# Kernel tuning notes

Measured on AMD Instinct MI355X. Metric: run time of the kernel, lower is better.

## Reference

```python
import jax, jax.numpy as jnp
import numpy as np

K_NEIGHBORS = 32  # nsample

def setup_inputs() -> dict:
    key = jax.random.key(0)
    ks = jax.random.split(key, 16)
    B, C, N = 4, 3, 4096
    def w(k, shape):
        return jax.random.normal(k, shape, dtype=jnp.float32) * 0.05
    inp = {"x": jax.random.normal(ks[0], (B, C, N), dtype=jnp.float32)}
    # three scale MLPs share shapes -> stack along leading scale axis (s=3)
    inp["sW0"] = w(ks[1], (3, 64, 3));    inp["sb0"] = w(ks[2], (3, 64))
    inp["sW1"] = w(ks[3], (3, 64, 64));   inp["sb1"] = w(ks[4], (3, 64))
    inp["sW2"] = w(ks[5], (3, 128, 64));  inp["sb2"] = w(ks[6], (3, 128))
    inp["gW0"] = w(ks[7], (256, 384));    inp["gb0"] = w(ks[8], (256,))
    inp["gW1"] = w(ks[9], (1024, 256));   inp["gb1"] = w(ks[10], (1024,))
    inp["mW0"] = w(ks[11], (256, 1024));  inp["mb0"] = w(ks[12], (256,))
    inp["mW1"] = w(ks[13], (128, 256));   inp["mb1"] = w(ks[14], (128,))
    return inp

def _knn_idx(x, k):
    # x: [B, 3, N] channels-first points; k nearest neighbors excluding self
    pts = jnp.swapaxes(x, 1, 2)                       # [B, N, 3]
    sq = jnp.sum(pts * pts, axis=-1)                  # [B, N]
    d = sq[:, :, None] + sq[:, None, :] - 2.0 * jnp.einsum('bnc,bmc->bnm', pts, pts)
    _, idx = jax.lax.top_k(-d, k + 1)                 # nearest first (self at 0)
    return idx[:, :, 1:]                              # [B, N, k]

def reference(x, sW0, sb0, sW1, sb1, sW2, sb2, gW0, gb0, gW1, gb1, mW0, mb0, mW1, mb1):
    B, C, N = x.shape
    # radius is unused by sample_and_group_knn -> all three scales share knn idx
    idx = _knn_idx(x, K_NEIGHBORS)                    # [B, N, K]
    # gather: per-batch x[:, idx[b]] -> [B, C, N, K]
    g = jax.vmap(lambda xf, i: xf[:, i])(x, idx)
    # three shared-weight 1x1-conv MLPs, batched over scale axis s
    h = jax.nn.relu(jnp.einsum('bcnk,soc->sbonk', g, sW0) + sb0[:, None, :, None, None])
    h = jax.nn.relu(jnp.einsum('sbcnk,soc->sbonk', h, sW1) + sb1[:, None, :, None, None])
    h = jax.nn.relu(jnp.einsum('sbcnk,soc->sbonk', h, sW2) + sb2[:, None, :, None, None])
    p = jnp.max(h, axis=-1)                           # [3, B, 128, N] max over neighbors
    point = jnp.moveaxis(p, 0, 1).reshape(B, 3 * p.shape[2], N)  # concat scales -> [B, 384, N]
    gf = jax.nn.relu(jnp.einsum('bcn,oc->bon', point, gW0) + gb0[None, :, None])
    gf = jax.nn.relu(jnp.einsum('bcn,oc->bon', gf, gW1) + gb1[None, :, None])     # [B,1024,N]
    msf = jax.nn.relu(jnp.einsum('bcn,oc->bon', gf, mW0) + mb0[None, :, None])
    msf = jax.nn.relu(jnp.einsum('bcn,oc->bon', msf, mW1) + mb1[None, :, None])   # [B,128,N]
    global_feature = jnp.max(gf, axis=-1)             # [B, 1024]
    return (global_feature, msf)
```

## Files before the change

kernel.cpp:

```cpp
#include <hip/hip_runtime.h>
#include <hip/hip_bf16.h>

#define NPTS 4096
#define KNN  32

typedef __attribute__((ext_vector_type(8))) short short8;
typedef __attribute__((ext_vector_type(4))) float floatx4;
typedef unsigned short u16x2 __attribute__((ext_vector_type(2)));

__device__ __forceinline__ unsigned short f2bf(float f) {
    unsigned u = __float_as_uint(f);
    u = (u + 0x7FFFu + ((u >> 16) & 1u)) >> 16;
    return (unsigned short)u;
}

__global__ __launch_bounds__(256) void prep_all(
    const float* __restrict__ x, float4* __restrict__ pts4,
    const float* __restrict__ gW0, const float* __restrict__ gW1,
    const float* __restrict__ mW0, const float* __restrict__ mW1,
    const float* __restrict__ sW1, const float* __restrict__ sW2,
    unsigned short* __restrict__ Wb0, unsigned short* __restrict__ Wb1,
    unsigned short* __restrict__ Wb2, unsigned short* __restrict__ Wb3,
    unsigned short* __restrict__ Wb4, unsigned short* __restrict__ Wb5)
{
    const int blk = blockIdx.x, t = threadIdx.x;
    if (blk < 64) {
        const int i = blk * 256 + t;
        const int b = i >> 12, n = i & (NPTS - 1);
        const float* xb = x + (size_t)b * 3 * NPTS;
        const float qx = xb[n], qy = xb[NPTS + n], qz = xb[2 * NPTS + n];
        pts4[i] = make_float4(qx, qy, qz, qx * qx + qy * qy + qz * qz);
    } else {
        const int wi = (blk - 64) * 256 + t;
        float v; unsigned short* dst;
        if (wi < 98304)       { v = gW0[wi];          dst = Wb0 + wi; }
        else if (wi < 360448) { v = gW1[wi - 98304];  dst = Wb1 + (wi - 98304); }
        else if (wi < 622592) { v = mW0[wi - 360448]; dst = Wb2 + (wi - 360448); }
        else if (wi < 655360) { v = mW1[wi - 622592]; dst = Wb3 + (wi - 622592); }
        else if (wi < 667648) { v = sW1[wi - 655360]; dst = Wb4 + (wi - 655360); }
        else                  { v = sW2[wi - 667648]; dst = Wb5 + (wi - 667648); }
        *dst = f2bf(v);
    }
}

__global__ __launch_bounds__(256) void knn_kernel15(const float4* __restrict__ pts4,
                                                    int* __restrict__ knn_out)
{
    __shared__ unsigned sredA[2][4], sredB[2][4];
    __shared__ unsigned long long C2[2][256];
    __shared__ unsigned ccnt[2];

    const int t = threadIdx.x, wid = t >> 6, lane = t & 63;
    const int pr = blockIdx.x;
    const int b  = pr >> 11;
    const int qa = (pr & 2047) << 1;
    const int qb = qa + 1;
    const float4* P = pts4 + ((size_t)b << 12);
    const float4 sA = P[qa];
    const float4 sB = P[qb];

    if (t < 2) ccnt[t] = 0u;

    unsigned kA[16], kB[16];
    #pragma unroll
    for (int r = 0; r < 16; ++r) {
        const float4 c = P[(r << 8) + t];
        float dA = (sA.w + c.w) - 2.0f * (sA.x * c.x + sA.y * c.y + sA.z * c.z);
        float dB = (sB.w + c.w) - 2.0f * (sB.x * c.x + sB.y * c.y + sB.z * c.z);
        unsigned uA = __float_as_uint(dA), uB = __float_as_uint(dB);
        kA[r] = (uA & 0x80000000u) ? ~uA : (uA | 0x80000000u);
        kB[r] = (uB & 0x80000000u) ? ~uB : (uB | 0x80000000u);
    }

    int pp = 0;
    auto countLE2 = [&](unsigned ta, unsigned tb, unsigned& ga, unsigned& gb) {
        unsigned ca = 0, cb = 0;
        #pragma unroll
        for (int r = 0; r < 16; ++r) {
            ca += (unsigned)__popcll(__ballot(kA[r] <= ta));
            cb += (unsigned)__popcll(__ballot(kB[r] <= tb));
        }
        if (lane == 0) { sredA[pp & 1][wid] = ca; sredB[pp & 1][wid] = cb; }
        __syncthreads();
        ga = sredA[pp & 1][0] + sredA[pp & 1][1] +
             sredA[pp & 1][2] + sredA[pp & 1][3];
        gb = sredB[pp & 1][0] + sredB[pp & 1][1] +
             sredB[pp & 1][2] + sredB[pp & 1][3];
        ++pp;
    };

    unsigned loA = 0x100u, hiA = 0x1FEu, cHiA = 4096u;
    unsigned loB = 0x100u, hiB = 0x1FEu, cHiB = 4096u;
    for (int it = 0; it < 8; ++it) {
        const unsigned mA = (loA + hiA) >> 1;
        const unsigned mB = (loB + hiB) >> 1;
        unsigned ga, gb;
        countLE2((mA << 23) | 0x7FFFFFu, (mB << 23) | 0x7FFFFFu, ga, gb);
        if (ga >= 33u) { hiA = mA; cHiA = ga; } else loA = mA + 1u;
        if (gb >= 33u) { hiB = mB; cHiB = gb; } else loB = mB + 1u;
    }
    unsigned loKA = loA << 23, hiKA = (loA << 23) | 0x7FFFFFu, cFA = cHiA;
    unsigned loKB = loB << 23, hiKB = (loB << 23) | 0x7FFFFFu, cFB = cHiB;

    while (((cFA > 256u) && (loKA < hiKA)) || ((cFB > 256u) && (loKB < hiKB))) {
        const bool nA = (cFA > 256u) && (loKA < hiKA);
        const bool nB = (cFB > 256u) && (loKB < hiKB);
        const unsigned mA = nA ? (loKA + ((hiKA - loKA) >> 1)) : hiKA;
        const unsigned mB = nB ? (loKB + ((hiKB - loKB) >> 1)) : hiKB;
        unsigned ga, gb;
        countLE2(mA, mB, ga, gb);
        if (nA) { if (ga >= 33u) { hiKA = mA; cFA = ga; } else loKA = mA + 1u; }
        if (nB) { if (gb >= 33u) { hiKB = mB; cFB = gb; } else loKB = mB + 1u; }
    }
    const unsigned thrA = hiKA, thrB = hiKB;

    #pragma unroll
    for (int r = 0; r < 16; ++r) {
        if (kA[r] <= thrA) {
            unsigned p = atomicAdd(&ccnt[0], 1u);
            if (p < 256u)
                C2[0][p] = ((unsigned long long)kA[r] << 32) |
                           (unsigned)((r << 8) + t);
        }
        if (kB[r] <= thrB) {
            unsigned p = atomicAdd(&ccnt[1], 1u);
            if (p < 256u)
                C2[1][p] = ((unsigned long long)kB[r] << 32) |
                           (unsigned)((r << 8) + t);
        }
    }
    __syncthreads();

    int ncA = (int)ccnt[0]; if (ncA > 256) ncA = 256;
    int ncB = (int)ccnt[1]; if (ncB > 256) ncB = 256;
    if (t < ncA) {
        const unsigned long long me = C2[0][t];
        int rank = 0;
        for (int j = 0; j < ncA; ++j) rank += (C2[0][j] < me) ? 1 : 0;
        if (rank >= 1 && rank <= KNN)
            knn_out[((size_t)((b << 12) + qa)) * KNN + (rank - 1)] =
                (int)(me & 0xFFFFFFFFu);
    }
    if (t < ncB) {
        const unsigned long long me = C2[1][t];
        int rank = 0;
        for (int j = 0; j < ncB; ++j) rank += (C2[1][j] < me) ? 1 : 0;
        if (rank >= 1 && rank <= KNN)
            knn_out[((size_t)((b << 12) + qb)) * KNN + (rank - 1)] =
                (int)(me & 0xFFFFFFFFu);
    }
}

__global__ __launch_bounds__(256) void pointmlp_mfma(
    const float* __restrict__ x,
    const float* __restrict__ sW0, const float* __restrict__ sb0,
    const unsigned short* __restrict__ W1b, const float* __restrict__ sb1,
    const unsigned short* __restrict__ W2b, const float* __restrict__ sb2,
    unsigned short* __restrict__ F)
{
    __shared__ __align__(16) unsigned short W1s[64 * 72];
    __shared__ __align__(16) unsigned short W2s[128 * 72];
    __shared__ __align__(16) unsigned short h0T[32 * 72];
    __shared__ __align__(16) unsigned short h1T[32 * 72];
    __shared__ float W0s[192];
    __shared__ float b0s[64], b1s[64], b2s[128];
    __shared__ float pts[3 * 33];

    const int t = threadIdx.x;
    const int s = blockIdx.y;
    const int tile = blockIdx.x;
    const int b = tile >> 7;
    const int j0 = (tile & 127) << 5;
    const float* xb = x + (size_t)b * 3 * NPTS;

    if (t < 192) W0s[t] = sW0[s * 192 + t];
    if (t < 64) b0s[t] = sb0[s * 64 + t];
    if (t >= 64 && t < 128) b1s[t - 64] = sb1[s * 64 + (t - 64)];
    if (t < 128) b2s[t] = sb2[s * 128 + t];
    if (t < 96) { int c = t >> 5, p = t & 31; pts[c * 33 + p] = xb[c * NPTS + j0 + p]; }
    {
        const int o = t & 63, qq = t >> 6;
        const unsigned short* src = W1b + (size_t)s * 4096 + o * 64 + qq * 16;
        *(uint4*)&W1s[o * 72 + qq * 16]     = *(const uint4*)src;
        *(uint4*)&W1s[o * 72 + qq * 16 + 8] = *(const uint4*)(src + 8);
    }
    {
        const int o2 = t & 127, hh = t >> 7;
        const unsigned short* src = W2b + (size_t)s * 8192 + o2 * 64 + hh * 32;
        *(uint4*)&W2s[o2 * 72 + hh * 32]      = *(const uint4*)src;
        *(uint4*)&W2s[o2 * 72 + hh * 32 + 8]  = *(const uint4*)(src + 8);
        *(uint4*)&W2s[o2 * 72 + hh * 32 + 16] = *(const uint4*)(src + 16);
        *(uint4*)&W2s[o2 * 72 + hh * 32 + 24] = *(const uint4*)(src + 24);
    }
    __syncthreads();

    {
        const int p = t & 31, og = t >> 5;
        const float xx = pts[p], yy = pts[33 + p], zz = pts[66 + p];
        unsigned short hv[8];
        #pragma unroll
        for (int r = 0; r < 8; ++r) {
            const int o = og * 8 + r;
            float a = b0s[o] + W0s[o * 3] * xx + W0s[o * 3 + 1] * yy
                    + W0s[o * 3 + 2] * zz;
            hv[r] = f2bf(fmaxf(a, 0.0f));
        }
        *(uint4*)&h0T[p * 72 + og * 8] = *(const uint4*)hv;
    }
    __syncthreads();

    const int w = t >> 6, lane = t & 63, quad = lane >> 4, l15 = lane & 15;

    {
        #pragma unroll
        for (int ni = 0; ni < 2; ++ni) {
            floatx4 acc = (floatx4){0.f, 0.f, 0.f, 0.f};
            #pragma unroll
            for (int k0 = 0; k0 < 2; ++k0) {
                short8 aF = *(const short8*)&W1s[(w * 16 + l15) * 72 + k0 * 32 + quad * 8];
                short8 bF = *(const short8*)&h0T[(ni * 16 + l15) * 72 + k0 * 32 + quad * 8];
                acc = __builtin_amdgcn_mfma_f32_16x16x32_bf16(aF, bF, acc, 0, 0, 0);
            }
            const int m0 = w * 16 + quad * 4;
            const int p = ni * 16 + l15;
            ushort4 pk;
            pk.x = f2bf(fmaxf(acc[0] + b1s[m0 + 0], 0.f));
            pk.y = f2bf(fmaxf(acc[1] + b1s[m0 + 1], 0.f));
            pk.z = f2bf(fmaxf(acc[2] + b1s[m0 + 2], 0.f));
            pk.w = f2bf(fmaxf(acc[3] + b1s[m0 + 3], 0.f));
            *(ushort4*)&h1T[p * 72 + m0] = pk;
        }
    }
    __syncthreads();

    {
        #pragma unroll
        for (int mi = 0; mi < 2; ++mi) {
            const int m0 = (w * 2 + mi) * 16;
            #pragma unroll
            for (int ni = 0; ni < 2; ++ni) {
                floatx4 acc = (floatx4){0.f, 0.f, 0.f, 0.f};
                #pragma unroll
                for (int k0 = 0; k0 < 2; ++k0) {
                    short8 aF = *(const short8*)&W2s[(m0 + l15) * 72 + k0 * 32 + quad * 8];
                    short8 bF = *(const short8*)&h1T[(ni * 16 + l15) * 72 + k0 * 32 + quad * 8];
                    acc = __builtin_amdgcn_mfma_f32_16x16x32_bf16(aF, bF, acc, 0, 0, 0);
                }
                const int o2 = m0 + quad * 4;
                const int j = j0 + ni * 16 + l15;
                ushort4 pk;
                pk.x = f2bf(fmaxf(acc[0] + b2s[o2 + 0], 0.f));
                pk.y = f2bf(fmaxf(acc[1] + b2s[o2 + 1], 0.f));
                pk.z = f2bf(fmaxf(acc[2] + b2s[o2 + 2], 0.f));
                pk.w = f2bf(fmaxf(acc[3] + b2s[o2 + 3], 0.f));
                *(ushort4*)&F[((size_t)b * NPTS + j) * 384 + s * 128 + o2] = pk;
            }
        }
    }
}

__global__ __launch_bounds__(192) void maxgather_bf16(
    const unsigned short* __restrict__ F, const int* __restrict__ knn,
    unsigned short* __restrict__ pt)
{
    __shared__ int idxS[KNN];
    const int q = blockIdx.x;
    const int b = q >> 12;
    const int t = threadIdx.x;
    if (t < KNN) idxS[t] = knn[(size_t)q * KNN + t];
    __syncthreads();
    const unsigned short* Fb = F + (size_t)b * NPTS * 384 + t * 2;
    u16x2 m = (u16x2)0;
    #pragma unroll 8
    for (int k = 0; k < KNN; ++k) {
        u16x2 v = *(const u16x2*)(Fb + (size_t)idxS[k] * 384);
        m = __builtin_elementwise_max(m, v);
    }
    *(u16x2*)(pt + (size_t)q * 384 + t * 2) = m;
}

template<int DO_ROWMAX>
__global__ __launch_bounds__(256) void gemm_bf16(
    const unsigned short* __restrict__ Wb, const unsigned short* __restrict__ Bt,
    const float* __restrict__ bias, void* __restrict__ outp,
    float* __restrict__ gfeat, int M, int K)
{
    __shared__ __align__(16) unsigned short As[128 * 40];
    __shared__ __align__(16) unsigned short Bs[128 * 40];
    __shared__ float biasS[128];
    __shared__ int redI[128];

    const int t = threadIdx.x;
    const int b = blockIdx.z;
    const int m0 = blockIdx.x * 128;
    const int n0 = blockIdx.y * 128;
    if (t < 128) biasS[t] = bias[m0 + t];
    if (DO_ROWMAX && t < 128) redI[t] = 0;

    const int wave = t >> 6, lane = t & 63, quad = lane >> 4, l15 = lane & 15;
    const int wr = wave >> 1, wc = wave & 1;

    const int am = t & 127, akh = t >> 7;
    const unsigned short* Wp = Wb + (size_t)(m0 + am) * K + akh * 16;
    const int bn = t >> 2, bq = t & 3;
    const unsigned short* Bp = Bt + ((size_t)b * NPTS + n0) * K;

    floatx4 acc[16];
    #pragma unroll
    for (int i = 0; i < 16; ++i) acc[i] = (floatx4){0.f, 0.f, 0.f, 0.f};

    const int nk = K >> 5;
    for (int kt = 0; kt < nk; ++kt) {
        const int k0 = kt << 5;
        uint4 av0 = *(const uint4*)(Wp + k0);
        uint4 av1 = *(const uint4*)(Wp + k0 + 8);
        uint4 bv0 = *(const uint4*)(Bp + (size_t)bn * K + k0 + bq * 8);
        uint4 bv1 = *(const uint4*)(Bp + (size_t)(bn + 64) * K + k0 + bq * 8);
        __syncthreads();
        {
            uint4* dst = (uint4*)&As[am * 40 + akh * 16];
            dst[0] = av0;
            dst[1] = av1;
            *(uint4*)&Bs[bn * 40 + bq * 8] = bv0;
            *(uint4*)&Bs[(bn + 64) * 40 + bq * 8] = bv1;
        }
        __syncthreads();
        short8 af[4], bfv[4];
        #pragma unroll
        for (int i = 0; i < 4; ++i)
            af[i] = *(const short8*)&As[(wr * 64 + i * 16 + l15) * 40 + quad * 8];
        #pragma unroll
        for (int j = 0; j < 4; ++j)
            bfv[j] = *(const short8*)&Bs[(wc * 64 + j * 16 + l15) * 40 + quad * 8];
        #pragma unroll
        for (int i = 0; i < 4; ++i)
            #pragma unroll
            for (int j = 0; j < 4; ++j)
                acc[i * 4 + j] = __builtin_amdgcn_mfma_f32_16x16x32_bf16(
                    af[i], bfv[j], acc[i * 4 + j], 0, 0, 0);
    }

    #pragma unroll
    for (int i = 0; i < 4; ++i) {
        const int mbase = wr * 64 + i * 16 + quad * 4;
        float rm0 = 0.f, rm1 = 0.f, rm2 = 0.f, rm3 = 0.f;
        #pragma unroll
        for (int j = 0; j < 4; ++j) {
            const int n = n0 + wc * 64 + j * 16 + l15;
            float v0 = fmaxf(acc[i * 4 + j][0] + biasS[mbase + 0], 0.f);
            float v1 = fmaxf(acc[i * 4 + j][1] + biasS[mbase + 1], 0.f);
            float v2 = fmaxf(acc[i * 4 + j][2] + biasS[mbase + 2], 0.f);
            float v3 = fmaxf(acc[i * 4 + j][3] + biasS[mbase + 3], 0.f);
            if (DO_ROWMAX) {
                rm0 = fmaxf(rm0, v0); rm1 = fmaxf(rm1, v1);
                rm2 = fmaxf(rm2, v2); rm3 = fmaxf(rm3, v3);
            }
            ushort4 pk;
            pk.x = f2bf(v0); pk.y = f2bf(v1); pk.z = f2bf(v2); pk.w = f2bf(v3);
            *(ushort4*)((unsigned short*)outp +
                        ((size_t)b * NPTS + n) * M + m0 + mbase) = pk;
        }
        if (DO_ROWMAX) {
            atomicMax(&redI[mbase + 0], __float_as_int(rm0));
            atomicMax(&redI[mbase + 1], __float_as_int(rm1));
            atomicMax(&redI[mbase + 2], __float_as_int(rm2));
            atomicMax(&redI[mbase + 3], __float_as_int(rm3));
        }
    }
    if (DO_ROWMAX) {
        __syncthreads();
        if (t < 128)
            atomicMax((int*)&gfeat[(size_t)b * 1024 + m0 + t], redI[t]);
    }
}

__global__ __launch_bounds__(256) void fused_head(
    const unsigned short* __restrict__ Wb2, const unsigned short* __restrict__ Wb3,
    const float* __restrict__ mb0, const float* __restrict__ mb1,
    const unsigned short* __restrict__ gft, float* __restrict__ outp)
{
    __shared__ __align__(16) unsigned short As[256 * 40];
    __shared__ __align__(16) unsigned short Bs[64 * 40];
    __shared__ __align__(16) unsigned short H[64 * 264];
    __shared__ float b0s[256];
    __shared__ float b1s[128];

    const int t = threadIdx.x;
    const int n0 = blockIdx.x * 64;
    const int b = blockIdx.y;
    b0s[t] = mb0[t];
    if (t < 128) b1s[t] = mb1[t];

    const int wave = t >> 6, lane = t & 63, quad = lane >> 4, l15 = lane & 15;

    const unsigned short* Ap = Wb2 + (size_t)t * 1024;
    const int bn = t >> 2, bq = t & 3;
    const unsigned short* Bp = gft + ((size_t)b * NPTS + n0) * 1024;

    floatx4 acc[16];
    #pragma unroll
    for (int i = 0; i < 16; ++i) acc[i] = (floatx4){0.f, 0.f, 0.f, 0.f};

    for (int kt = 0; kt < 32; ++kt) {
        const int k0 = kt << 5;
        uint4 a0 = *(const uint4*)(Ap + k0);
        uint4 a1 = *(const uint4*)(Ap + k0 + 8);
        uint4 a2 = *(const uint4*)(Ap + k0 + 16);
        uint4 a3 = *(const uint4*)(Ap + k0 + 24);
        uint4 bv = *(const uint4*)(Bp + (size_t)bn * 1024 + k0 + bq * 8);
        __syncthreads();
        *(uint4*)&As[t * 40 + 0]  = a0;
        *(uint4*)&As[t * 40 + 8]  = a1;
        *(uint4*)&As[t * 40 + 16] = a2;
        *(uint4*)&As[t * 40 + 24] = a3;
        *(uint4*)&Bs[bn * 40 + bq * 8] = bv;
        __syncthreads();
        short8 af[4], bfv[4];
        #pragma unroll
        for (int i = 0; i < 4; ++i)
            af[i] = *(const short8*)&As[(wave * 64 + i * 16 + l15) * 40 + quad * 8];
        #pragma unroll
        for (int j = 0; j < 4; ++j)
            bfv[j] = *(const short8*)&Bs[(j * 16 + l15) * 40 + quad * 8];
        #pragma unroll
        for (int i = 0; i < 4; ++i)
            #pragma unroll
            for (int j = 0; j < 4; ++j)
                acc[i * 4 + j] = __builtin_amdgcn_mfma_f32_16x16x32_bf16(
                    af[i], bfv[j], acc[i * 4 + j], 0, 0, 0);
    }
    #pragma unroll
    for (int i = 0; i < 4; ++i) {
        const int mbase = wave * 64 + i * 16 + quad * 4;
        #pragma unroll
        for (int j = 0; j < 4; ++j) {
            const int nl = j * 16 + l15;
            ushort4 pk;
            pk.x = f2bf(fmaxf(acc[i * 4 + j][0] + b0s[mbase + 0], 0.f));
            pk.y = f2bf(fmaxf(acc[i * 4 + j][1] + b0s[mbase + 1], 0.f));
            pk.z = f2bf(fmaxf(acc[i * 4 + j][2] + b0s[mbase + 2], 0.f));
            pk.w = f2bf(fmaxf(acc[i * 4 + j][3] + b0s[mbase + 3], 0.f));
            *(ushort4*)&H[nl * 264 + mbase] = pk;
        }
    }

    floatx4 acc2[8];
    #pragma unroll
    for (int i = 0; i < 8; ++i) acc2[i] = (floatx4){0.f, 0.f, 0.f, 0.f};
    const int am2 = t & 127, ah = t >> 7;

    for (int kt = 0; kt < 8; ++kt) {
        const int k0 = kt << 5;
        uint4 a0 = *(const uint4*)(Wb3 + (size_t)am2 * 256 + k0 + ah * 16);
        uint4 a1 = *(const uint4*)(Wb3 + (size_t)am2 * 256 + k0 + ah * 16 + 8);
        __syncthreads();
        *(uint4*)&As[am2 * 40 + ah * 16]     = a0;
        *(uint4*)&As[am2 * 40 + ah * 16 + 8] = a1;
        __syncthreads();
        short8 af2[2], bf2[4];
        #pragma unroll
        for (int i = 0; i < 2; ++i)
            af2[i] = *(const short8*)&As[(wave * 32 + i * 16 + l15) * 40 + quad * 8];
        #pragma unroll
        for (int j = 0; j < 4; ++j)
            bf2[j] = *(const short8*)&H[(j * 16 + l15) * 264 + k0 + quad * 8];
        #pragma unroll
        for (int i = 0; i < 2; ++i)
            #pragma unroll
            for (int j = 0; j < 4; ++j)
                acc2[i * 4 + j] = __builtin_amdgcn_mfma_f32_16x16x32_bf16(
                    af2[i], bf2[j], acc2[i * 4 + j], 0, 0, 0);
    }
    #pragma unroll
    for (int i = 0; i < 2; ++i) {
        const int m2 = wave * 32 + i * 16 + quad * 4;
        #pragma unroll
        for (int j = 0; j < 4; ++j) {
            const int n = n0 + j * 16 + l15;
            float* o = outp + ((size_t)b * 128 + m2) * NPTS + n;
            o[0 * NPTS] = fmaxf(acc2[i * 4 + j][0] + b1s[m2 + 0], 0.f);
            o[1 * NPTS] = fmaxf(acc2[i * 4 + j][1] + b1s[m2 + 1], 0.f);
            o[2 * NPTS] = fmaxf(acc2[i * 4 + j][2] + b1s[m2 + 2], 0.f);
            o[3 * NPTS] = fmaxf(acc2[i * 4 + j][3] + b1s[m2 + 3], 0.f);
        }
    }
}

extern "C" void kernel_launch(void* const* d_in, const int* in_sizes, int n_in,
                              void* d_out, int out_size, void* d_ws, size_t ws_size,
                              hipStream_t stream)
{
    const float* x   = (const float*)d_in[0];
    const float* sW0 = (const float*)d_in[1];
    const float* sb0 = (const float*)d_in[2];
    const float* sW1 = (const float*)d_in[3];
    const float* sb1 = (const float*)d_in[4];
    const float* sW2 = (const float*)d_in[5];
    const float* sb2 = (const float*)d_in[6];
    const float* gW0 = (const float*)d_in[7];
    const float* gb0 = (const float*)d_in[8];
    const float* gW1 = (const float*)d_in[9];
    const float* gb1 = (const float*)d_in[10];
    const float* mW0 = (const float*)d_in[11];
    const float* mb0 = (const float*)d_in[12];
    const float* mW1 = (const float*)d_in[13];
    const float* mb1 = (const float*)d_in[14];
    float* outp = (float*)d_out;

    char* ws = (char*)d_ws;
    int*            idx     = (int*)(ws);
    float4*         pts4    = (float4*)(ws + 2097152u);
    unsigned short* Wb0     = (unsigned short*)(ws + 2359296u);
    unsigned short* Wb1     = (unsigned short*)(ws + 2555904u);
    unsigned short* Wb2     = (unsigned short*)(ws + 3080192u);
    unsigned short* Wb3     = (unsigned short*)(ws + 3604480u);
    unsigned short* Wb4     = (unsigned short*)(ws + 3670016u);
    unsigned short* Wb5     = (unsigned short*)(ws + 3694592u);
    unsigned short* F       = (unsigned short*)(ws + 4194304u);
    unsigned short* point_t = (unsigned short*)(ws + 18874368u);
    unsigned short* gf0t    = (unsigned short*)(ws + 33554432u);
    unsigned short* gft     = (unsigned short*)(ws + 50331648u);

    prep_all<<<dim3(2768), dim3(256), 0, stream>>>(
        x, pts4, gW0, gW1, mW0, mW1, sW1, sW2, Wb0, Wb1, Wb2, Wb3, Wb4, Wb5);
    knn_kernel15<<<dim3(8192), dim3(256), 0, stream>>>(pts4, idx);
    pointmlp_mfma<<<dim3(512, 3), dim3(256), 0, stream>>>(
        x, sW0, sb0, Wb4, sb1, Wb5, sb2, F);
    maxgather_bf16<<<dim3(16384), dim3(192), 0, stream>>>(F, idx, point_t);
    gemm_bf16<0><<<dim3(2, 32, 4), dim3(256), 0, stream>>>(
        Wb0, point_t, gb0, gf0t, nullptr, 256, 384);
    gemm_bf16<1><<<dim3(8, 32, 4), dim3(256), 0, stream>>>(
        Wb1, gf0t, gb1, gft, outp, 1024, 256);
    fused_head<<<dim3(64, 4), dim3(256), 0, stream>>>(
        Wb2, Wb3, mb0, mb1, gft, outp + 4096);
}
```

Measured before the change: 277.5 us.

## Pick kNN threshold from per-thread minima instead of iterated block-wide binary search

The kNN kernel takes each thread's minimum key, reduces these to 64 per-lane minima, and binary-searches the top 16 key bits within a single wavefront using ballots. That gives a candidate threshold without repeated block-wide __syncthreads count passes. If more than 256 candidates pass, it falls back to the old two-phase search, and when both candidate sets fit in 64 it uses a fixed 64-wide rank loop on separate wavefronts. The threshold is guaranteed to keep at least 33 elements, but how tight it is depends on the point distribution, so the fallback may run often.

```diff
diff --git a/kernel.cpp b/kernel.cpp
--- a/kernel.cpp
+++ b/kernel.cpp
@@ -43,111 +43,201 @@
     }
 }
 
-__global__ __launch_bounds__(256) void knn_kernel15(const float4* __restrict__ pts4,
+__global__ __launch_bounds__(256) void knn_kernel19(const float4* __restrict__ pts4,
                                                     int* __restrict__ knn_out)
 {
     __shared__ unsigned sredA[2][4], sredB[2][4];
-    __shared__ unsigned long long C2[2][256];
-    __shared__ unsigned ccnt[2];
+    __shared__ unsigned minSA[256], minSB[256];
+    __shared__ unsigned long long CA[256], CB[256];
+    __shared__ unsigned ccnt2[2];
 
     const int t = threadIdx.x, wid = t >> 6, lane = t & 63;
     const int pr = blockIdx.x;
     const int b  = pr >> 11;
-    const int qa = (pr & 2047) << 1;
+    const int qa = ((pr & 2047) << 1);
     const int qb = qa + 1;
     const float4* P = pts4 + ((size_t)b << 12);
     const float4 sA = P[qa];
     const float4 sB = P[qb];
 
-    if (t < 2) ccnt[t] = 0u;
+    if (t < 2) ccnt2[t] = 0u;
+    CA[t] = 0xFFFFFFFFFFFFFFFFULL;
+    CB[t] = 0xFFFFFFFFFFFFFFFFULL;
 
     unsigned kA[16], kB[16];
     #pragma unroll
-    for (int r = 0; r < 16; ++r) {
-        const float4 c = P[(r << 8) + t];
-        float dA = (sA.w + c.w) - 2.0f * (sA.x * c.x + sA.y * c.y + sA.z * c.z);
-        float dB = (sB.w + c.w) - 2.0f * (sB.x * c.x + sB.y * c.y + sB.z * c.z);
-        unsigned uA = __float_as_uint(dA), uB = __float_as_uint(dB);
-        kA[r] = (uA & 0x80000000u) ? ~uA : (uA | 0x80000000u);
-        kB[r] = (uB & 0x80000000u) ? ~uB : (uB | 0x80000000u);
-    }
-
-    int pp = 0;
-    auto countLE2 = [&](unsigned ta, unsigned tb, unsigned& ga, unsigned& gb) {
-        unsigned ca = 0, cb = 0;
-        #pragma unroll
-        for (int r = 0; r < 16; ++r) {
-            ca += (unsigned)__popcll(__ballot(kA[r] <= ta));
-            cb += (unsigned)__popcll(__ballot(kB[r] <= tb));
-        }
-        if (lane == 0) { sredA[pp & 1][wid] = ca; sredB[pp & 1][wid] = cb; }
-        __syncthreads();
-        ga = sredA[pp & 1][0] + sredA[pp & 1][1] +
-             sredA[pp & 1][2] + sredA[pp & 1][3];
-        gb = sredB[pp & 1][0] + sredB[pp & 1][1] +
-             sredB[pp & 1][2] + sredB[pp & 1][3];
-        ++pp;
-    };
-
-    unsigned loA = 0x100u, hiA = 0x1FEu, cHiA = 4096u;
-    unsigned loB = 0x100u, hiB = 0x1FEu, cHiB = 4096u;
-    for (int it = 0; it < 8; ++it) {
-        const unsigned mA = (loA + hiA) >> 1;
-        const unsigned mB = (loB + hiB) >> 1;
-        unsigned ga, gb;
-        countLE2((mA << 23) | 0x7FFFFFu, (mB << 23) | 0x7FFFFFu, ga, gb);
-        if (ga >= 33u) { hiA = mA; cHiA = ga; } else loA = mA + 1u;
-        if (gb >= 33u) { hiB = mB; cHiB = gb; } else loB = mB + 1u;
-    }
-    unsigned loKA = loA << 23, hiKA = (loA << 23) | 0x7FFFFFu, cFA = cHiA;
-    unsigned loKB = loB << 23, hiKB = (loB << 23) | 0x7FFFFFu, cFB = cHiB;
-
-    while (((cFA > 256u) && (loKA < hiKA)) || ((cFB > 256u) && (loKB < hiKB))) {
-        const bool nA = (cFA > 256u) && (loKA < hiKA);
-        const bool nB = (cFB > 256u) && (loKB < hiKB);
-        const unsigned mA = nA ? (loKA + ((hiKA - loKA) >> 1)) : hiKA;
-        const unsigned mB = nB ? (loKB + ((hiKB - loKB) >> 1)) : hiKB;
-        unsigned ga, gb;
-        countLE2(mA, mB, ga, gb);
-        if (nA) { if (ga >= 33u) { hiKA = mA; cFA = ga; } else loKA = mA + 1u; }
-        if (nB) { if (gb >= 33u) { hiKB = mB; cFB = gb; } else loKB = mB + 1u; }
-    }
-    const unsigned thrA = hiKA, thrB = hiKB;
+    for (int g = 0; g < 4; ++g) {
+        float4 c0 = P[((g * 4 + 0) << 8) + t];
+        float4 c1 = P[((g * 4 + 1) << 8) + t];
+        float4 c2 = P[((g * 4 + 2) << 8) + t];
+        float4 c3 = P[((g * 4 + 3) << 8) + t];
+        float dA0 = (sA.w + c0.w) - 2.0f * (sA.x * c0.x + sA.y * c0.y + sA.z * c0.z);
+        float dA1 = (sA.w + c1.w) - 2.0f * (sA.x * c1.x + sA.y * c1.y + sA.z * c1.z);
+        float dA2 = (sA.w + c2.w) - 2.0f * (sA.x * c2.x + sA.y * c2.y + sA.z * c2.z);
+        float dA3 = (sA.w + c3.w) - 2.0f * (sA.x * c3.x + sA.y * c3.y + sA.z * c3.z);
+        float dB0 = (sB.w + c0.w) - 2.0f * (sB.x * c0.x + sB.y * c0.y + sB.z * c0.z);
+        float dB1 = (sB.w + c1.w) - 2.0f * (sB.x * c1.x + sB.y * c1.y + sB.z * c1.z);
+        float dB2 = (sB.w + c2.w) - 2.0f * (sB.x * c2.x + sB.y * c2.y + sB.z * c2.z);
+        float dB3 = (sB.w + c3.w) - 2.0f * (sB.x * c3.x + sB.y * c3.y + sB.z * c3.z);
+        unsigned uA0 = __float_as_uint(dA0), uA1 = __float_as_uint(dA1);
+        unsigned uA2 = __float_as_uint(dA2), uA3 = __float_as_uint(dA3);
+        unsigned uB0 = __float_as_uint(dB0), uB1 = __float_as_uint(dB1);
+        unsigned uB2 = __float_as_uint(dB2), uB3 = __float_as_uint(dB3);
+        kA[g * 4 + 0] = uA0 ^ (((unsigned)((int)uA0 >> 31)) | 0x80000000u);
+        kA[g * 4 + 1] = uA1 ^ (((unsigned)((int)uA1 >> 31)) | 0x80000000u);
+        kA[g * 4 + 2] = uA2 ^ (((unsigned)((int)uA2 >> 31)) | 0x80000000u);
+        kA[g * 4 + 3] = uA3 ^ (((unsigned)((int)uA3 >> 31)) | 0x80000000u);
+        kB[g * 4 + 0] = uB0 ^ (((unsigned)((int)uB0 >> 31)) | 0x80000000u);
+        kB[g * 4 + 1] = uB1 ^ (((unsigned)((int)uB1 >> 31)) | 0x80000000u);
+        kB[g * 4 + 2] = uB2 ^ (((unsigned)((int)uB2 >> 31)) | 0x80000000u);
+        kB[g * 4 + 3] = uB3 ^ (((unsigned)((int)uB3 >> 31)) | 0x80000000u);
+    }
+
+    unsigned tmA = kA[0], tmB = kB[0];
+    #pragma unroll
+    for (int r = 1; r < 16; ++r) {
+        tmA = (kA[r] < tmA) ? kA[r] : tmA;
+        tmB = (kB[r] < tmB) ? kB[r] : tmB;
+    }
+    minSA[t] = tmA;
+    minSB[t] = tmB;
+    __syncthreads();
+
+    unsigned mA = minSA[lane], mB = minSB[lane];
+    {
+        unsigned a1 = minSA[lane + 64], a2 = minSA[lane + 128], a3 = minSA[lane + 192];
+        unsigned b1 = minSB[lane + 64], b2 = minSB[lane + 128], b3 = minSB[lane + 192];
+        mA = (a1 < mA) ? a1 : mA;  a2 = (a3 < a2) ? a3 : a2;  mA = (a2 < mA) ? a2 : mA;
+        mB = (b1 < mB) ? b1 : mB;  b2 = (b3 < b2) ? b3 : b2;  mB = (b2 < mB) ? b2 : mB;
+    }
+
+    const unsigned msA = mA >> 16, msB = mB >> 16;
+    unsigned loA = 0u, hiA = 0xFFFFu, loB = 0u, hiB = 0xFFFFu;
+    for (int i = 0; i < 16; ++i) {
+        const unsigned midA = (loA + hiA) >> 1;
+        const unsigned midB = (loB + hiB) >> 1;
+        const unsigned cA = (unsigned)__popcll(__ballot(msA <= midA));
+        const unsigned cB = (unsigned)__popcll(__ballot(msB <= midB));
+        if (cA >= 33u) hiA = midA; else loA = midA + 1u;
+        if (cB >= 33u) hiB = midB; else loB = midB + 1u;
+    }
+    const unsigned thrA = (hiA << 16) | 0xFFFFu;
+    const unsigned thrB = (hiB << 16) | 0xFFFFu;
 
     #pragma unroll
     for (int r = 0; r < 16; ++r) {
         if (kA[r] <= thrA) {
-            unsigned p = atomicAdd(&ccnt[0], 1u);
+            unsigned p = atomicAdd(&ccnt2[0], 1u);
             if (p < 256u)
-                C2[0][p] = ((unsigned long long)kA[r] << 32) |
-                           (unsigned)((r << 8) + t);
+                CA[p] = ((unsigned long long)kA[r] << 32) | (unsigned)((r << 8) + t);
         }
         if (kB[r] <= thrB) {
-            unsigned p = atomicAdd(&ccnt[1], 1u);
+            unsigned p = atomicAdd(&ccnt2[1], 1u);
             if (p < 256u)
-                C2[1][p] = ((unsigned long long)kB[r] << 32) |
-                           (unsigned)((r << 8) + t);
+                CB[p] = ((unsigned long long)kB[r] << 32) | (unsigned)((r << 8) + t);
         }
     }
     __syncthreads();
 
-    int ncA = (int)ccnt[0]; if (ncA > 256) ncA = 256;
-    int ncB = (int)ccnt[1]; if (ncB > 256) ncB = 256;
-    if (t < ncA) {
-        const unsigned long long me = C2[0][t];
-        int rank = 0;
-        for (int j = 0; j < ncA; ++j) rank += (C2[0][j] < me) ? 1 : 0;
-        if (rank >= 1 && rank <= KNN)
-            knn_out[((size_t)((b << 12) + qa)) * KNN + (rank - 1)] =
-                (int)(me & 0xFFFFFFFFu);
-    }
-    if (t < ncB) {
-        const unsigned long long me = C2[1][t];
-        int rank = 0;
-        for (int j = 0; j < ncB; ++j) rank += (C2[1][j] < me) ? 1 : 0;
-        if (rank >= 1 && rank <= KNN)
-            knn_out[((size_t)((b << 12) + qb)) * KNN + (rank - 1)] =
-                (int)(me & 0xFFFFFFFFu);
+    int ncA = (int)ccnt2[0];
+    int ncB = (int)ccnt2[1];
+    bool fell_back = false;
+    if (ncA > 256 || ncB > 256) {
+        fell_back = true;
+        if (t < 2) ccnt2[t] = 0u;
+        int pp = 0;
+        auto countLE2 = [&](unsigned ta, unsigned tb, unsigned& ga, unsigned& gb) {
+            unsigned ca = 0, cb = 0;
+            #pragma unroll
+            for (int r = 0; r < 16; ++r) {
+                ca += (unsigned)__popcll(__ballot(kA[r] <= ta));
+                cb += (unsigned)__popcll(__ballot(kB[r] <= tb));
+            }
+            if (lane == 0) { sredA[pp & 1][wid] = ca; sredB[pp & 1][wid] = cb; }
+            __syncthreads();
+            ga = sredA[pp & 1][0] + sredA[pp & 1][1] +
+                 sredA[pp & 1][2] + sredA[pp & 1][3];
+            gb = sredB[pp & 1][0] + sredB[pp & 1][1] +
+                 sredB[pp & 1][2] + sredB[pp & 1][3];
+            ++pp;
+        };
+        unsigned lo2A = 0x100u, hi2A = 0x1FEu, cHiA = 4096u;
+        unsigned lo2B = 0x100u, hi2B = 0x1FEu, cHiB = 4096u;
+        for (int it = 0; it < 8; ++it) {
+            const unsigned mAe = (lo2A + hi2A) >> 1;
+            const unsigned mBe = (lo2B + hi2B) >> 1;
+            unsigned ga, gb;
+            countLE2((mAe << 23) | 0x7FFFFFu, (mBe << 23) | 0x7FFFFFu, ga, gb);
+            if (ga >= 33u) { hi2A = mAe; cHiA = ga; } else lo2A = mAe + 1u;
+            if (gb >= 33u) { hi2B = mBe; cHiB = gb; } else lo2B = mBe + 1u;
+        }
+        unsigned loKA = lo2A << 23, hiKA = (lo2A << 23) | 0x7FFFFFu, cFA = cHiA;
+        unsigned loKB = lo2B << 23, hiKB = (lo2B << 23) | 0x7FFFFFu, cFB = cHiB;
+        while (((cFA > 256u) && (loKA < hiKA)) || ((cFB > 256u) && (loKB < hiKB))) {
+            const bool nAx = (cFA > 256u) && (loKA < hiKA);
+            const bool nBx = (cFB > 256u) && (loKB < hiKB);
+            const unsigned mAk = nAx ? (loKA + ((hiKA - loKA) >> 1)) : hiKA;
+            const unsigned mBk = nBx ? (loKB + ((hiKB - loKB) >> 1)) : hiKB;
+            unsigned ga, gb;
+            countLE2(mAk, mBk, ga, gb);
+            if (nAx) { if (ga >= 33u) { hiKA = mAk; cFA = ga; } else loKA = mAk + 1u; }
+            if (nBx) { if (gb >= 33u) { hiKB = mBk; cFB = gb; } else loKB = mBk + 1u; }
+        }
+        const unsigned tFA = hiKA, tFB = hiKB;
+        #pragma unroll
+        for (int r = 0; r < 16; ++r) {
+            if (kA[r] <= tFA) {
+                unsigned p = atomicAdd(&ccnt2[0], 1u);
+                if (p < 256u)
+                    CA[p] = ((unsigned long long)kA[r] << 32) | (unsigned)((r << 8) + t);
+            }
+            if (kB[r] <= tFB) {
+                unsigned p = atomicAdd(&ccnt2[1], 1u);
+                if (p < 256u)
+                    CB[p] = ((unsigned long long)kB[r] << 32) | (unsigned)((r << 8) + t);
+            }
+        }
+        __syncthreads();
+        ncA = (int)ccnt2[0]; if (ncA > 256) ncA = 256;
+        ncB = (int)ccnt2[1]; if (ncB > 256) ncB = 256;
+    }
+
+    if (!fell_back && ncA <= 64 && ncB <= 64) {
+        if (t < 64) {
+            const unsigned long long me = CA[t];
+            int rank = 0;
+            #pragma unroll
+            for (int j = 0; j < 64; ++j) rank += (CA[j] < me) ? 1 : 0;
+            if (rank >= 1 && rank <= KNN)
+                knn_out[((size_t)((b << 12) + qa)) * KNN + (rank - 1)] =
+                    (int)(me & 0xFFFFFFFFu);
+        } else if (t < 128) {
+            const int tb = t - 64;
+            const unsigned long long me = CB[tb];
+            int rank = 0;
+            #pragma unroll
+            for (int j = 0; j < 64; ++j) rank += (CB[j] < me) ? 1 : 0;
+            if (rank >= 1 && rank <= KNN)
+                knn_out[((size_t)((b << 12) + qb)) * KNN + (rank - 1)] =
+                    (int)(me & 0xFFFFFFFFu);
+        }
+    } else {
+        if (t < ncA) {
+            const unsigned long long me = CA[t];
+            int rank = 0;
+            for (int j = 0; j < ncA; ++j) rank += (CA[j] < me) ? 1 : 0;
+            if (rank >= 1 && rank <= KNN)
+                knn_out[((size_t)((b << 12) + qa)) * KNN + (rank - 1)] =
+                    (int)(me & 0xFFFFFFFFu);
+        }
+        if (t < ncB) {
+            const unsigned long long me = CB[t];
+            int rank = 0;
+            for (int j = 0; j < ncB; ++j) rank += (CB[j] < me) ? 1 : 0;
+            if (rank >= 1 && rank <= KNN)
+                knn_out[((size_t)((b << 12) + qb)) * KNN + (rank - 1)] =
+                    (int)(me & 0xFFFFFFFFu);
+        }
     }
 }
 
@@ -523,7 +613,7 @@
 
     prep_all<<<dim3(2768), dim3(256), 0, stream>>>(
         x, pts4, gW0, gW1, mW0, mW1, sW1, sW2, Wb0, Wb1, Wb2, Wb3, Wb4, Wb5);
-    knn_kernel15<<<dim3(8192), dim3(256), 0, stream>>>(pts4, idx);
+    knn_kernel19<<<dim3(8192), dim3(256), 0, stream>>>(pts4, idx);
     pointmlp_mfma<<<dim3(512, 3), dim3(256), 0, stream>>>(
         x, sW0, sb0, Wb4, sb1, Wb5, sb2, F);
     maxgather_bf16<<<dim3(16384), dim3(192), 0, stream>>>(F, idx, point_t);
```

After: 240.8 us. -13.2%, faster.
